# Kernel tuning notes

Hardware: AMD Instinct MI355X
Metric: run time of the kernel (lower is better)

Reference implementation:

```python
import math
import jax, jax.numpy as jnp
import numpy as np

S, M, B, NH, HD = 512, 512, 8, 16, 64  # SentenceLength, MemoryLength, BatchSize, heads, head_size
H = NH * HD   # 1024 hidden
K = M + S     # key length = r_length
LAYERS, TOTAL_LEN = 2, 1536


def setup_inputs() -> dict:
    key = jax.random.key(0)
    ks = jax.random.split(key, 12)
    w = lambda k: jax.random.normal(k, (H, H), jnp.float32) * 0.02
    return {
        "x": jax.random.normal(ks[0], (B, S, H), jnp.float32),
        "rel_pos_emb": jax.random.normal(ks[1], (K, H), jnp.float32),
        "attention_mask": jnp.ones((B, S), jnp.float32),  # unused by the original forward
        "memories": jax.random.normal(ks[2], (LAYERS, B, TOTAL_LEN, H), jnp.float32),
        "Wq": w(ks[3]), "Wke": w(ks[4]), "Wv": w(ks[5]), "Wkr": w(ks[6]),
        "u": jax.random.normal(ks[7], (NH, HD), jnp.float32),
        "v": jax.random.normal(ks[8], (NH, HD), jnp.float32),
        "Wo": w(ks[9]),
        "bo": jnp.zeros((H,), jnp.float32),
        "layer_num": 0,
        "segment_num": 0,
    }


def rel_shift(bd):
    # Vectorized form of the original per-row loop:
    # row qi keeps bd[qi][qlen-1-qi:] and zero-pads the tail.
    qlen, klen = bd.shape[0], bd.shape[1]
    shift = (qlen - 1) - jnp.arange(qlen)            # [qlen]
    idx = shift[:, None] + jnp.arange(klen)[None, :]  # [qlen, klen]
    valid = (idx < klen)
    idx_c = jnp.minimum(idx, klen - 1)
    out = bd[jnp.arange(qlen)[:, None], idx_c]        # gather along key axis
    return out * valid[:, :, None, None].astype(bd.dtype)


def reference(x, rel_pos_emb, attention_mask, memories, Wq, Wke, Wv, Wkr, u, v, Wo, bo, layer_num, segment_num):
    # memory segment for this layer: [B, M, H]
    sg_m = memories[layer_num, :, segment_num * M:(segment_num + 1) * M, :]
    kvx = jnp.concatenate([sg_m, x], axis=1)          # [B, K, H]
    # Projections, then the original's raw .view() reinterpretation (not a transpose)
    qx = (x.reshape(-1, H) @ Wq).reshape(S, B, NH, HD)
    kx = (kvx.reshape(-1, H) @ Wke).reshape(K, B, NH, HD)
    vx = (kvx.reshape(-1, H) @ Wv).reshape(K, B, NH, HD)
    kr = (rel_pos_emb @ Wkr).reshape(K, NH, HD)
    ac = jnp.einsum('ibnd,jbnd->ijbn', qx + u, kx)    # content score [S,K,B,NH]
    bd = jnp.einsum('ibnd,jnd->ijbn', qx + v, kr)     # position score
    bd = rel_shift(bd)
    att = (ac + bd) / math.sqrt(float(HD))
    att = jax.nn.softmax(att, axis=-1)                # original uses Softmax(dim=-1) on [i,j,b,n]
    out = jnp.einsum('ijbn,jbnd->ibnd', att, vx)      # [S,B,NH,HD]
    out = out.reshape(B, S, H)                        # original's raw contiguous().view()
    out = out @ Wo + bo                               # o_dense (dropout is identity in eval)
    # update_memories_by_layer (no_grad in torch -> stop_gradient here)
    new_mem = memories.at[layer_num, :, segment_num * S + M:(segment_num + 1) * S + M, :].set(
        jax.lax.stop_gradient(out))
    return out, new_mem
```

## Files before the change

### kernel.cpp

```cpp
#include <hip/hip_runtime.h>
#include <hip/hip_bf16.h>

#define OUT_OFF 4194304
#define NM_ELEMS 25165824

typedef __attribute__((ext_vector_type(8))) short short8;
typedef __attribute__((ext_vector_type(4))) float f32x4;

static __device__ __forceinline__ float4 ld4(const float* p) {
  return *reinterpret_cast<const float4*>(p);
}
static __device__ __forceinline__ short bfbits(float f) {
  __hip_bfloat16 h = __float2bfloat16(f);
  return *reinterpret_cast<short*>(&h);
}
static __device__ __forceinline__ void gload16(const void* g, void* l) {
  __builtin_amdgcn_global_load_lds(
      (const __attribute__((address_space(1))) void*)g,
      (__attribute__((address_space(3))) void*)l, 16, 0, 0);
}

__global__ __launch_bounds__(256)
void cw_k(const float* __restrict__ W0, const float* __restrict__ W1,
          const float* __restrict__ W2, const float* __restrict__ W3,
          const float* __restrict__ W4,
          __hip_bfloat16* __restrict__ T0, __hip_bfloat16* __restrict__ T1,
          __hip_bfloat16* __restrict__ T2, __hip_bfloat16* __restrict__ T3,
          __hip_bfloat16* __restrict__ T4)
{
  const float* W; __hip_bfloat16* T;
  switch (blockIdx.z) {
    case 0: W = W0; T = T0; break;
    case 1: W = W1; T = T1; break;
    case 2: W = W2; T = T2; break;
    case 3: W = W3; T = T3; break;
    default: W = W4; T = T4; break;
  }
  __shared__ short S[64][72];
  const int t = threadIdx.x;
  const int n0 = blockIdx.x * 64, k0 = blockIdx.y * 64;
  #pragma unroll
  for (int it = 0; it < 2; ++it) {
    const int kl = (t >> 3) + it * 32;
    const int n8 = (t & 7) * 8;
    const float* src = W + (size_t)(k0 + kl) * 1024 + n0 + n8;
    const float4 f0 = ld4(src), f1 = ld4(src + 4);
    short8 s;
    s[0]=bfbits(f0.x); s[1]=bfbits(f0.y); s[2]=bfbits(f0.z); s[3]=bfbits(f0.w);
    s[4]=bfbits(f1.x); s[5]=bfbits(f1.y); s[6]=bfbits(f1.z); s[7]=bfbits(f1.w);
    *reinterpret_cast<short8*>(&S[kl][n8]) = s;
  }
  __syncthreads();
  #pragma unroll
  for (int it = 0; it < 2; ++it) {
    const int nl = (t >> 3) + it * 32;
    const int k8 = (t & 7) * 8;
    short8 s;
    #pragma unroll
    for (int e = 0; e < 8; ++e) s[e] = S[k8 + e][nl];
    *reinterpret_cast<short8*>((short*)T + (size_t)(n0 + nl) * 1024 + k0 + k8) = s;
  }
}

__global__ __launch_bounds__(256)
void ckvx_k(const float* __restrict__ x, const float* __restrict__ mem,
            const int* __restrict__ lp, const int* __restrict__ sp,
            __hip_bfloat16* __restrict__ Kvx)
{
  const size_t t = (size_t)blockIdx.x * 256 + threadIdx.x;
  const int r = (int)(t >> 7);
  const int c = (int)(t & 127) * 8;
  const int b = r >> 10, j = r & 1023;
  const float* src = (j < 512)
    ? mem + (((size_t)lp[0] * 8 + b) * 1536 + (size_t)sp[0] * 512 + j) * 1024 + c
    : x + ((size_t)b * 512 + (j - 512)) * 1024 + c;
  const float4 f0 = ld4(src), f1 = ld4(src + 4);
  short8 s;
  s[0]=bfbits(f0.x); s[1]=bfbits(f0.y); s[2]=bfbits(f0.z); s[3]=bfbits(f0.w);
  s[4]=bfbits(f1.x); s[5]=bfbits(f1.y); s[6]=bfbits(f1.z); s[7]=bfbits(f1.w);
  *reinterpret_cast<short8*>((short*)Kvx + (size_t)r * 1024 + c) = s;
}

__global__ __launch_bounds__(256)
void crpe_k(const float* __restrict__ R, __hip_bfloat16* __restrict__ Rb)
{
  const size_t t = ((size_t)blockIdx.x * 256 + threadIdx.x) * 8;
  const float4 f0 = ld4(R + t), f1 = ld4(R + t + 4);
  short8 s;
  s[0]=bfbits(f0.x); s[1]=bfbits(f0.y); s[2]=bfbits(f0.z); s[3]=bfbits(f0.w);
  s[4]=bfbits(f1.x); s[5]=bfbits(f1.y); s[6]=bfbits(f1.z); s[7]=bfbits(f1.w);
  *reinterpret_cast<short8*>((short*)Rb + t) = s;
}

template<int MODE>
__global__ __launch_bounds__(256)
void mgemm(const __hip_bfloat16* __restrict__ A,
           const __hip_bfloat16* __restrict__ Wt,
           const float* __restrict__ P0, const float* __restrict__ P1,
           const int* __restrict__ lp, const int* __restrict__ sp,
           __hip_bfloat16* __restrict__ Cb, __hip_bfloat16* __restrict__ Cb2,
           float* __restrict__ C)
{
  __shared__ __align__(16) short As[128 * 64];
  __shared__ __align__(16) short Bs[128 * 64];
  const int tid = threadIdx.x;
  const int w   = tid >> 6;
  const int l   = tid & 63;
  const int l15 = l & 15, lg = l >> 4;
  const int m0 = blockIdx.y * 128;
  const int n0 = blockIdx.x * 128;
  const int wr = (w >> 1) * 64;
  const int wc = (w & 1) * 64;

  f32x4 acc[4][4];
  #pragma unroll
  for (int mi = 0; mi < 4; ++mi)
    #pragma unroll
    for (int ni = 0; ni < 4; ++ni) acc[mi][ni] = (f32x4){0.f, 0.f, 0.f, 0.f};

  const int srow = (l >> 3);
  const int scol = (l & 7) * 8;

  for (int k0 = 0; k0 < 1024; k0 += 64) {
    if (k0) __syncthreads();
    #pragma unroll
    for (int q = 0; q < 4; ++q) {
      const int seg = w * 32 + q * 8;
      const int ra = m0 + seg + srow;
      size_t aoff;
      if (MODE == 4)
        aoff = ((size_t)(ra >> 9) * 1024 + 512 + (ra & 511)) * 1024;
      else
        aoff = (size_t)ra * 1024;
      gload16((const short*)A + aoff + k0 + scol, &As[seg * 64]);
      const int rb = n0 + seg + srow;
      gload16((const short*)Wt + (size_t)rb * 1024 + k0 + scol, &Bs[seg * 64]);
    }
    __syncthreads();
    #pragma unroll
    for (int kk = 0; kk < 2; ++kk) {
      short8 a[4], bf[4];
      #pragma unroll
      for (int mi = 0; mi < 4; ++mi)
        a[mi] = *reinterpret_cast<const short8*>(
            &As[(wr + mi * 16 + l15) * 64 + kk * 32 + lg * 8]);
      #pragma unroll
      for (int ni = 0; ni < 4; ++ni)
        bf[ni] = *reinterpret_cast<const short8*>(
            &Bs[(wc + ni * 16 + l15) * 64 + kk * 32 + lg * 8]);
      #pragma unroll
      for (int mi = 0; mi < 4; ++mi)
        #pragma unroll
        for (int ni = 0; ni < 4; ++ni)
          acc[mi][ni] = __builtin_amdgcn_mfma_f32_16x16x32_bf16(
              a[mi], bf[ni], acc[mi][ni], 0, 0, 0);
    }
  }

  #pragma unroll
  for (int mi = 0; mi < 4; ++mi) {
    const int rbase = m0 + wr + mi * 16 + lg * 4;
    #pragma unroll
    for (int ni = 0; ni < 4; ++ni) {
      const int col = n0 + wc + ni * 16 + l15;
      const int nh = col >> 6, dd = col & 63;
      #pragma unroll
      for (int rr = 0; rr < 4; ++rr) {
        const int row = rbase + rr;
        const float val = acc[mi][ni][rr];
        if (MODE == 3) {
          Cb[(size_t)row * 1024 + col] = __float2bfloat16(val);
        } else if (MODE == 4) {
          const int i = row >> 3, bb = row & 7;
          const size_t o = (((size_t)(bb * 16 + nh) * 512) + i) * 64 + dd;
          Cb [o] = __float2bfloat16(val + P0[col]);
          Cb2[o] = __float2bfloat16(val + P1[col]);
        } else if (MODE == 5) {
          const int j = row >> 3, bb = row & 7;
          Cb[(((size_t)(bb * 16 + nh) * 1024) + j) * 64 + dd] =
              __float2bfloat16(val);
        } else if (MODE == 2) {
          const float o = val + P0[col];
          C[(size_t)row * 1024 + col] = o;
          const int b2 = row >> 9, s2 = row & 511;
          C[OUT_OFF +
            (((size_t)lp[0] * 8 + b2) * 1536 + 512 + (size_t)sp[0] * 512 + s2) *
                1024 + col] = o;
        }
      }
    }
  }
}

__global__ __launch_bounds__(256)
void tr_k(const __hip_bfloat16* __restrict__ VE, __hip_bfloat16* __restrict__ Vt)
{
  __shared__ short T[64][72];
  const int t = threadIdx.x;
  const int j0 = blockIdx.x * 64;
  const int bn = blockIdx.y;
  #pragma unroll
  for (int it = 0; it < 2; ++it) {
    const int jl = (t >> 3) + it * 32;
    const int d8 = (t & 7) * 8;
    *reinterpret_cast<short8*>(&T[jl][d8]) =
        *reinterpret_cast<const short8*>(
            (const short*)VE + ((size_t)bn * 1024 + j0 + jl) * 64 + d8);
  }
  __syncthreads();
  #pragma unroll
  for (int it = 0; it < 2; ++it) {
    const int dl = (t >> 3) + it * 32;
    const int j8 = (t & 7) * 8;
    short8 s;
    #pragma unroll
    for (int e = 0; e < 8; ++e) s[e] = T[j8 + e][dl];
    *reinterpret_cast<short8*>(
        (short*)Vt + ((size_t)bn * 64 + dl) * 1024 + j0 + j8) = s;
  }
}

__global__ __launch_bounds__(512, 1)
void attn2(const __hip_bfloat16* __restrict__ QU, const __hip_bfloat16* __restrict__ QV,
           const __hip_bfloat16* __restrict__ KE, const __hip_bfloat16* __restrict__ Vt,
           const __hip_bfloat16* __restrict__ KR, __hip_bfloat16* __restrict__ Ob)
{
  __shared__ __align__(16) short stg[49152];
  __shared__ float Lbuf[16*16*17];
  __shared__ __hip_bfloat16 Abuf[16*16*36];

  const int bid = blockIdx.x;
  const int b   = bid & 7;
  const int i0  = (bid >> 3) * 16;
  const int tid = threadIdx.x;
  const int w   = tid >> 6;
  const int l   = tid & 63;
  const int l15 = l & 15;
  const int lg  = l >> 4;

  short* keW = stg + w * 6144;
  short* krW = keW + 2048;

  const short* KEs = (const short*)KE;
  const short* KRs = (const short*)KR;

  short8 qu[2][2], qv[2][2];
  #pragma unroll
  for (int hh = 0; hh < 2; ++hh) {
    const int h = 2*w + hh;
    const size_t qb = (((size_t)(b*16 + h) * 512) + i0 + l15) * 64 + lg*8;
    #pragma unroll
    for (int kf = 0; kf < 2; ++kf) {
      qu[hh][kf] = *reinterpret_cast<const short8*>(QU + qb + kf*32);
      qv[hh][kf] = *reinterpret_cast<const short8*>(QV + qb + kf*32);
    }
  }

  f32x4 oacc[2][4];
  #pragma unroll
  for (int hh = 0; hh < 2; ++hh)
    #pragma unroll
    for (int nf = 0; nf < 4; ++nf) oacc[hh][nf] = (f32x4){0.f,0.f,0.f,0.f};

  auto stage = [&](int j0) {
    const int pb = 496 - i0 + j0;
    #pragma unroll
    for (int q = 0; q < 4; ++q) {
      const int R  = q*8 + (l >> 3);
      const int hh = R >> 4, jl = R & 15;
      const int c  = (l & 7) ^ (R & 7);
      gload16(KEs + (((size_t)(b*16 + 2*w + hh) * 1024) + j0 + jl) * 64 + c * 8,
              keW + q * 512);
    }
    #pragma unroll
    for (int q = 0; q < 8; ++q) {
      const int r = q*4 + (l >> 4);
      const int c = (l & 15) ^ (r & 15);
      gload16(KRs + ((size_t)(pb + r)) * 1024 + w * 128 + c * 8,
              krW + q * 512);
    }
  };

  stage(0);

  for (int pr = 0; pr < 32; ++pr) {
    const int j0e = pr * 32;
    short8 vb[2][4];

    #pragma unroll
    for (int half = 0; half < 2; ++half) {
      const int j0 = j0e + half * 16;

      asm volatile("s_waitcnt vmcnt(0)" ::: "memory");
      __builtin_amdgcn_sched_barrier(0);

      short8 kef[2][2], krf[2][2][2];
      #pragma unroll
      for (int hh = 0; hh < 2; ++hh)
        #pragma unroll
        for (int kf = 0; kf < 2; ++kf) {
          const int rowE = hh*16 + l15;
          const int kcE  = (kf*4 + lg) ^ (rowE & 7);
          kef[hh][kf] = *reinterpret_cast<const short8*>(
              keW + rowE*64 + kcE*8);
          #pragma unroll
          for (int nf = 0; nf < 2; ++nf) {
            const int rowR = nf*16 + l15;
            const int kcR  = (hh*8 + kf*4 + lg) ^ (rowR & 15);
            krf[hh][nf][kf] = *reinterpret_cast<const short8*>(
                krW + rowR*128 + kcR*8);
          }
        }

      __builtin_amdgcn_s_setprio(1);
      f32x4 ac[2], tf[2][2];
      #pragma unroll
      for (int hh = 0; hh < 2; ++hh) {
        ac[hh]    = (f32x4){0,0,0,0};
        tf[hh][0] = (f32x4){0,0,0,0};
        tf[hh][1] = (f32x4){0,0,0,0};
        #pragma unroll
        for (int kf = 0; kf < 2; ++kf) {
          ac[hh] = __builtin_amdgcn_mfma_f32_16x16x32_bf16(
              qu[hh][kf], kef[hh][kf], ac[hh], 0, 0, 0);
          #pragma unroll
          for (int nf = 0; nf < 2; ++nf)
            tf[hh][nf] = __builtin_amdgcn_mfma_f32_16x16x32_bf16(
                qv[hh][kf], krf[hh][nf][kf], tf[hh][nf], 0, 0, 0);
        }
      }
      __builtin_amdgcn_s_setprio(0);

      asm volatile("s_waitcnt lgkmcnt(0)" ::: "memory");
      __builtin_amdgcn_sched_barrier(0);
      stage(j0 + 16);
      if (half == 0) {
        #pragma unroll
        for (int hh = 0; hh < 2; ++hh) {
          const int h = 2*w + hh;
          #pragma unroll
          for (int nf = 0; nf < 4; ++nf)
            vb[hh][nf] = *reinterpret_cast<const short8*>(
              Vt + (((size_t)(b*16 + h) * 64) + nf*16 + l15) * 1024 + j0e + lg*8);
        }
      }

      #pragma unroll
      for (int hh = 0; hh < 2; ++hh) {
        const int h = 2*w + hh;
        #pragma unroll
        for (int r = 0; r < 4; ++r) {
          const int ip  = lg*4 + r;
          const int idx = 15 - ip + l15;
          const int nf  = idx >> 4;
          const int Ls  = lg*16 + (idx & 15);
          const float v0 = __shfl(tf[hh][0][r], Ls, 64);
          const float v1 = __shfl(tf[hh][1][r], Ls, 64);
          const float bd = nf ? v1 : v0;
          Lbuf[(h*16 + ip)*17 + l15] = 0.125f * (ac[hh][r] + bd);
        }
      }
      __syncthreads();

      if (tid < 256) {
        const int si = tid >> 4, sj = tid & 15;
        float vals[16];
        float m = -3.0e38f;
        #pragma unroll
        for (int n = 0; n < 16; ++n) {
          vals[n] = Lbuf[(n*16 + si)*17 + sj];
          m = fmaxf(m, vals[n]);
        }
        float s = 0.f;
        #pragma unroll
        for (int n = 0; n < 16; ++n) { vals[n] = __expf(vals[n] - m); s += vals[n]; }
        const float rinv = 1.0f / s;
        #pragma unroll
        for (int n = 0; n < 16; ++n)
          Abuf[(n*16 + si)*36 + half*16 + sj] = __float2bfloat16(vals[n] * rinv);
      }
      __syncthreads();

      if (half == 1) {
        __builtin_amdgcn_s_setprio(1);
        #pragma unroll
        for (int hh = 0; hh < 2; ++hh) {
          const int h = 2*w + hh;
          const short8 af = *reinterpret_cast<const short8*>(
              &Abuf[(h*16 + l15)*36 + lg*8]);
          #pragma unroll
          for (int nf = 0; nf < 4; ++nf)
            oacc[hh][nf] = __builtin_amdgcn_mfma_f32_16x16x32_bf16(
                af, vb[hh][nf], oacc[hh][nf], 0, 0, 0);
        }
        __builtin_amdgcn_s_setprio(0);
      }
    }
  }

  #pragma unroll
  for (int hh = 0; hh < 2; ++hh) {
    const int h = 2*w + hh;
    #pragma unroll
    for (int nf = 0; nf < 4; ++nf)
      #pragma unroll
      for (int r = 0; r < 4; ++r) {
        const int i = i0 + lg*4 + r;
        Ob[((size_t)(i*8 + b)) * 1024 + h*64 + nf*16 + l15] =
            __float2bfloat16(oacc[hh][nf][r]);
      }
  }
}

extern "C" void kernel_launch(void* const* d_in, const int* in_sizes, int n_in,
                              void* d_out, int out_size, void* d_ws, size_t ws_size,
                              hipStream_t stream)
{
  const float* x   = (const float*)d_in[0];
  const float* rpe = (const float*)d_in[1];
  const float* mem = (const float*)d_in[3];
  const float* Wq  = (const float*)d_in[4];
  const float* Wke = (const float*)d_in[5];
  const float* Wv  = (const float*)d_in[6];
  const float* Wkr = (const float*)d_in[7];
  const float* u   = (const float*)d_in[8];
  const float* v   = (const float*)d_in[9];
  const float* Wo  = (const float*)d_in[10];
  const float* bo  = (const float*)d_in[11];
  const int* lp    = (const int*)d_in[12];
  const int* sp    = (const int*)d_in[13];

  float* out = (float*)d_out;
  float* nm  = out + OUT_OFF;

  float* ws = (float*)d_ws;
  __hip_bfloat16* QUb = (__hip_bfloat16*)(ws);
  __hip_bfloat16* QVb = (__hip_bfloat16*)(ws + 2097152);
  __hip_bfloat16* KRb = (__hip_bfloat16*)(ws + 4194304);
  __hip_bfloat16* Ob  = (__hip_bfloat16*)(ws + 4980736);
  __hip_bfloat16* Rb  = (__hip_bfloat16*)(ws + 7077888);
  __hip_bfloat16* WtO = (__hip_bfloat16*)(ws + 7602176);
  __hip_bfloat16* Kvx = (__hip_bfloat16*)(nm);
  __hip_bfloat16* KEb = (__hip_bfloat16*)(nm + 4194304);
  __hip_bfloat16* VEb = (__hip_bfloat16*)(nm + 8388608);
  __hip_bfloat16* Vtb = (__hip_bfloat16*)(nm + 12582912);
  __hip_bfloat16* WtQ = (__hip_bfloat16*)(nm + 16777216);
  __hip_bfloat16* WtK = (__hip_bfloat16*)(nm + 17301504);
  __hip_bfloat16* WtV = (__hip_bfloat16*)(nm + 17825792);
  __hip_bfloat16* WtR = (__hip_bfloat16*)(nm + 18350080);

  dim3 blk(256);
  hipMemsetAsync((void*)(KRb + (size_t)1024*1024), 0, (size_t)512*1024*2, stream);

  cw_k <<<dim3(16,16,5), blk, 0, stream>>>(Wq, Wke, Wv, Wkr, Wo,
                                           WtQ, WtK, WtV, WtR, WtO);
  ckvx_k<<<4096, blk, 0, stream>>>(x, mem, lp, sp, Kvx);
  crpe_k<<<512,  blk, 0, stream>>>(rpe, Rb);

  mgemm<3><<<dim3(8, 8),  blk, 0, stream>>>(Rb,  WtR, nullptr, nullptr, lp, sp, KRb, nullptr, nullptr);
  mgemm<4><<<dim3(8, 32), blk, 0, stream>>>(Kvx, WtQ, u, v,             lp, sp, QUb, QVb,     nullptr);
  mgemm<5><<<dim3(8, 64), blk, 0, stream>>>(Kvx, WtK, nullptr, nullptr, lp, sp, KEb, nullptr, nullptr);
  mgemm<5><<<dim3(8, 64), blk, 0, stream>>>(Kvx, WtV, nullptr, nullptr, lp, sp, VEb, nullptr, nullptr);

  tr_k<<<dim3(16, 128), blk, 0, stream>>>(VEb, Vtb);

  attn2<<<dim3(256), dim3(512), 0, stream>>>(QUb, QVb, KEb, Vtb, KRb, Ob);

  hipMemcpyAsync(nm, mem, (size_t)NM_ELEMS * 4ull, hipMemcpyDeviceToDevice, stream);

  mgemm<2><<<dim3(8, 32), blk, 0, stream>>>(Ob, WtO, bo, nullptr, lp, sp, nullptr, nullptr, out);
}
```

Measured before the change: 382.4 us.

## Use one wave per head in attention and fuse K/V projection GEMMs

The attention kernel now launches 1024 threads per block, so each of the 16 waves handles a single head instead of two. This halves per-wave register and LDS staging and gives more waves to hide latency. The separate K and V projection GEMMs are merged into one MODE 7 launch over a doubled N range, with the destination picked by column. The merge relies on WtK and WtV sitting next to each other in the workspace, and the larger block raises register pressure limits.

After: 390.4 us. 2.1% more time.

```diff
diff --git a/kernel.cpp b/kernel.cpp
--- a/kernel.cpp
+++ b/kernel.cpp
@@ -163,7 +163,6 @@
     #pragma unroll
     for (int ni = 0; ni < 4; ++ni) {
       const int col = n0 + wc + ni * 16 + l15;
-      const int nh = col >> 6, dd = col & 63;
       #pragma unroll
       for (int rr = 0; rr < 4; ++rr) {
         const int row = rbase + rr;
@@ -171,13 +170,17 @@
         if (MODE == 3) {
           Cb[(size_t)row * 1024 + col] = __float2bfloat16(val);
         } else if (MODE == 4) {
+          const int nh = col >> 6, dd = col & 63;
           const int i = row >> 3, bb = row & 7;
           const size_t o = (((size_t)(bb * 16 + nh) * 512) + i) * 64 + dd;
           Cb [o] = __float2bfloat16(val + P0[col]);
           Cb2[o] = __float2bfloat16(val + P1[col]);
-        } else if (MODE == 5) {
+        } else if (MODE == 7) {
+          const int cc = col & 1023;
+          const int nh = cc >> 6, dd = cc & 63;
           const int j = row >> 3, bb = row & 7;
-          Cb[(((size_t)(bb * 16 + nh) * 1024) + j) * 64 + dd] =
+          __hip_bfloat16* dst = (col < 1024) ? Cb : Cb2;
+          dst[(((size_t)(bb * 16 + nh) * 1024) + j) * 64 + dd] =
               __float2bfloat16(val);
         } else if (MODE == 2) {
           const float o = val + P0[col];
@@ -220,7 +223,7 @@
   }
 }
 
-__global__ __launch_bounds__(512, 1)
+__global__ __launch_bounds__(1024, 4)
 void attn2(const __hip_bfloat16* __restrict__ QU, const __hip_bfloat16* __restrict__ QV,
            const __hip_bfloat16* __restrict__ KE, const __hip_bfloat16* __restrict__ Vt,
            const __hip_bfloat16* __restrict__ KR, __hip_bfloat16* __restrict__ Ob)
@@ -238,45 +241,40 @@
   const int l15 = l & 15;
   const int lg  = l >> 4;
 
-  short* keW = stg + w * 6144;
-  short* krW = keW + 2048;
+  short* keW = stg + w * 3072;
+  short* krW = keW + 1024;
 
   const short* KEs = (const short*)KE;
   const short* KRs = (const short*)KR;
 
-  short8 qu[2][2], qv[2][2];
-  #pragma unroll
-  for (int hh = 0; hh < 2; ++hh) {
-    const int h = 2*w + hh;
-    const size_t qb = (((size_t)(b*16 + h) * 512) + i0 + l15) * 64 + lg*8;
+  short8 qu[2], qv[2];
+  {
+    const size_t qb = (((size_t)(b*16 + w) * 512) + i0 + l15) * 64 + lg*8;
     #pragma unroll
     for (int kf = 0; kf < 2; ++kf) {
-      qu[hh][kf] = *reinterpret_cast<const short8*>(QU + qb + kf*32);
-      qv[hh][kf] = *reinterpret_cast<const short8*>(QV + qb + kf*32);
-    }
-  }
-
-  f32x4 oacc[2][4];
-  #pragma unroll
-  for (int hh = 0; hh < 2; ++hh)
-    #pragma unroll
-    for (int nf = 0; nf < 4; ++nf) oacc[hh][nf] = (f32x4){0.f,0.f,0.f,0.f};
+      qu[kf] = *reinterpret_cast<const short8*>(QU + qb + kf*32);
+      qv[kf] = *reinterpret_cast<const short8*>(QV + qb + kf*32);
+    }
+  }
+
+  f32x4 oacc[4];
+  #pragma unroll
+  for (int nf = 0; nf < 4; ++nf) oacc[nf] = (f32x4){0.f,0.f,0.f,0.f};
 
   auto stage = [&](int j0) {
     const int pb = 496 - i0 + j0;
     #pragma unroll
+    for (int q = 0; q < 2; ++q) {
+      const int R = q*8 + (l >> 3);
+      const int c = (l & 7) ^ (R & 7);
+      gload16(KEs + (((size_t)(b*16 + w) * 1024) + j0 + R) * 64 + c * 8,
+              keW + q * 512);
+    }
+    #pragma unroll
     for (int q = 0; q < 4; ++q) {
-      const int R  = q*8 + (l >> 3);
-      const int hh = R >> 4, jl = R & 15;
-      const int c  = (l & 7) ^ (R & 7);
-      gload16(KEs + (((size_t)(b*16 + 2*w + hh) * 1024) + j0 + jl) * 64 + c * 8,
-              keW + q * 512);
-    }
-    #pragma unroll
-    for (int q = 0; q < 8; ++q) {
-      const int r = q*4 + (l >> 4);
-      const int c = (l & 15) ^ (r & 15);
-      gload16(KRs + ((size_t)(pb + r)) * 1024 + w * 128 + c * 8,
+      const int r = q*8 + (l >> 3);
+      const int c = (l & 7) ^ (r & 7);
+      gload16(KRs + ((size_t)(pb + r)) * 1024 + w * 64 + c * 8,
               krW + q * 512);
     }
   };
@@ -285,7 +283,7 @@
 
   for (int pr = 0; pr < 32; ++pr) {
     const int j0e = pr * 32;
-    short8 vb[2][4];
+    short8 vb[4];
 
     #pragma unroll
     for (int half = 0; half < 2; ++half) {
@@ -294,40 +292,28 @@
       asm volatile("s_waitcnt vmcnt(0)" ::: "memory");
       __builtin_amdgcn_sched_barrier(0);
 
-      short8 kef[2][2], krf[2][2][2];
-      #pragma unroll
-      for (int hh = 0; hh < 2; ++hh)
-        #pragma unroll
-        for (int kf = 0; kf < 2; ++kf) {
-          const int rowE = hh*16 + l15;
-          const int kcE  = (kf*4 + lg) ^ (rowE & 7);
-          kef[hh][kf] = *reinterpret_cast<const short8*>(
-              keW + rowE*64 + kcE*8);
-          #pragma unroll
-          for (int nf = 0; nf < 2; ++nf) {
-            const int rowR = nf*16 + l15;
-            const int kcR  = (hh*8 + kf*4 + lg) ^ (rowR & 15);
-            krf[hh][nf][kf] = *reinterpret_cast<const short8*>(
-                krW + rowR*128 + kcR*8);
-          }
+      short8 kef[2], krf[2][2];
+      #pragma unroll
+      for (int kf = 0; kf < 2; ++kf) {
+        const int kcE = (kf*4 + lg) ^ (l15 & 7);
+        kef[kf] = *reinterpret_cast<const short8*>(keW + l15*64 + kcE*8);
+        #pragma unroll
+        for (int nf = 0; nf < 2; ++nf) {
+          const int rowR = nf*16 + l15;
+          const int kcR  = (kf*4 + lg) ^ (rowR & 7);
+          krf[nf][kf] = *reinterpret_cast<const short8*>(
+              krW + rowR*64 + kcR*8);
         }
+      }
 
       __builtin_amdgcn_s_setprio(1);
-      f32x4 ac[2], tf[2][2];
-      #pragma unroll
-      for (int hh = 0; hh < 2; ++hh) {
-        ac[hh]    = (f32x4){0,0,0,0};
-        tf[hh][0] = (f32x4){0,0,0,0};
-        tf[hh][1] = (f32x4){0,0,0,0};
-        #pragma unroll
-        for (int kf = 0; kf < 2; ++kf) {
-          ac[hh] = __builtin_amdgcn_mfma_f32_16x16x32_bf16(
-              qu[hh][kf], kef[hh][kf], ac[hh], 0, 0, 0);
-          #pragma unroll
-          for (int nf = 0; nf < 2; ++nf)
-            tf[hh][nf] = __builtin_amdgcn_mfma_f32_16x16x32_bf16(
-                qv[hh][kf], krf[hh][nf][kf], tf[hh][nf], 0, 0, 0);
-        }
+      f32x4 ac = (f32x4){0,0,0,0};
+      f32x4 tf0 = (f32x4){0,0,0,0}, tf1 = (f32x4){0,0,0,0};
+      #pragma unroll
+      for (int kf = 0; kf < 2; ++kf) {
+        ac  = __builtin_amdgcn_mfma_f32_16x16x32_bf16(qu[kf], kef[kf], ac, 0, 0, 0);
+        tf0 = __builtin_amdgcn_mfma_f32_16x16x32_bf16(qv[kf], krf[0][kf], tf0, 0, 0, 0);
+        tf1 = __builtin_amdgcn_mfma_f32_16x16x32_bf16(qv[kf], krf[1][kf], tf1, 0, 0, 0);
       }
       __builtin_amdgcn_s_setprio(0);
 
@@ -336,29 +322,21 @@
       stage(j0 + 16);
       if (half == 0) {
         #pragma unroll
-        for (int hh = 0; hh < 2; ++hh) {
-          const int h = 2*w + hh;
-          #pragma unroll
-          for (int nf = 0; nf < 4; ++nf)
-            vb[hh][nf] = *reinterpret_cast<const short8*>(
-              Vt + (((size_t)(b*16 + h) * 64) + nf*16 + l15) * 1024 + j0e + lg*8);
-        }
-      }
-
-      #pragma unroll
-      for (int hh = 0; hh < 2; ++hh) {
-        const int h = 2*w + hh;
-        #pragma unroll
-        for (int r = 0; r < 4; ++r) {
-          const int ip  = lg*4 + r;
-          const int idx = 15 - ip + l15;
-          const int nf  = idx >> 4;
-          const int Ls  = lg*16 + (idx & 15);
-          const float v0 = __shfl(tf[hh][0][r], Ls, 64);
-          const float v1 = __shfl(tf[hh][1][r], Ls, 64);
-          const float bd = nf ? v1 : v0;
-          Lbuf[(h*16 + ip)*17 + l15] = 0.125f * (ac[hh][r] + bd);
-        }
+        for (int nf = 0; nf < 4; ++nf)
+          vb[nf] = *reinterpret_cast<const short8*>(
+            Vt + (((size_t)(b*16 + w) * 64) + nf*16 + l15) * 1024 + j0e + lg*8);
+      }
+
+      #pragma unroll
+      for (int r = 0; r < 4; ++r) {
+        const int ip  = lg*4 + r;
+        const int idx = 15 - ip + l15;
+        const int nf  = idx >> 4;
+        const int Ls  = lg*16 + (idx & 15);
+        const float v0 = __shfl(tf0[r], Ls, 64);
+        const float v1 = __shfl(tf1[r], Ls, 64);
+        const float bd = nf ? v1 : v0;
+        Lbuf[(w*16 + ip)*17 + l15] = 0.125f * (ac[r] + bd);
       }
       __syncthreads();
 
@@ -383,33 +361,25 @@
 
       if (half == 1) {
         __builtin_amdgcn_s_setprio(1);
-        #pragma unroll
-        for (int hh = 0; hh < 2; ++hh) {
-          const int h = 2*w + hh;
-          const short8 af = *reinterpret_cast<const short8*>(
-              &Abuf[(h*16 + l15)*36 + lg*8]);
-          #pragma unroll
-          for (int nf = 0; nf < 4; ++nf)
-            oacc[hh][nf] = __builtin_amdgcn_mfma_f32_16x16x32_bf16(
-                af, vb[hh][nf], oacc[hh][nf], 0, 0, 0);
-        }
+        const short8 af = *reinterpret_cast<const short8*>(
+            &Abuf[(w*16 + l15)*36 + lg*8]);
+        #pragma unroll
+        for (int nf = 0; nf < 4; ++nf)
+          oacc[nf] = __builtin_amdgcn_mfma_f32_16x16x32_bf16(
+              af, vb[nf], oacc[nf], 0, 0, 0);
         __builtin_amdgcn_s_setprio(0);
       }
     }
   }
 
   #pragma unroll
-  for (int hh = 0; hh < 2; ++hh) {
-    const int h = 2*w + hh;
-    #pragma unroll
-    for (int nf = 0; nf < 4; ++nf)
-      #pragma unroll
-      for (int r = 0; r < 4; ++r) {
-        const int i = i0 + lg*4 + r;
-        Ob[((size_t)(i*8 + b)) * 1024 + h*64 + nf*16 + l15] =
-            __float2bfloat16(oacc[hh][nf][r]);
-      }
-  }
+  for (int nf = 0; nf < 4; ++nf)
+    #pragma unroll
+    for (int r = 0; r < 4; ++r) {
+      const int i = i0 + lg*4 + r;
+      Ob[((size_t)(i*8 + b)) * 1024 + w*64 + nf*16 + l15] =
+          __float2bfloat16(oacc[nf][r]);
+    }
 }
 
 extern "C" void kernel_launch(void* const* d_in, const int* in_sizes, int n_in,
@@ -459,12 +429,11 @@
 
   mgemm<3><<<dim3(8, 8),  blk, 0, stream>>>(Rb,  WtR, nullptr, nullptr, lp, sp, KRb, nullptr, nullptr);
   mgemm<4><<<dim3(8, 32), blk, 0, stream>>>(Kvx, WtQ, u, v,             lp, sp, QUb, QVb,     nullptr);
-  mgemm<5><<<dim3(8, 64), blk, 0, stream>>>(Kvx, WtK, nullptr, nullptr, lp, sp, KEb, nullptr, nullptr);
-  mgemm<5><<<dim3(8, 64), blk, 0, stream>>>(Kvx, WtV, nullptr, nullptr, lp, sp, VEb, nullptr, nullptr);
+  mgemm<7><<<dim3(16, 64), blk, 0, stream>>>(Kvx, WtK, nullptr, nullptr, lp, sp, KEb, VEb, nullptr);
 
   tr_k<<<dim3(16, 128), blk, 0, stream>>>(VEb, Vtb);
 
-  attn2<<<dim3(256), dim3(512), 0, stream>>>(QUb, QVb, KEb, Vtb, KRb, Ob);
+  attn2<<<dim3(256), dim3(1024), 0, stream>>>(QUb, QVb, KEb, Vtb, KRb, Ob);
 
   hipMemcpyAsync(nm, mem, (size_t)NM_ELEMS * 4ull, hipMemcpyDeviceToDevice, stream);
 
```
